# Optimization experiments

Hardware: AMD Instinct MI355X
Metric: run time of the kernel (lower is better)

Reference implementation:

```python
import jax, jax.numpy as jnp
import numpy as np

N = 20000      # nodes per snapshot
E = 160000     # edges per snapshot
T = 8          # timesteps
F_IN = 256     # nfeat
HEADS = 4      # GAT heads
C = 128        # nhid_graph (per-head GAT out, concat=False -> mean)
GH = 128       # nhid_gru
NC = 2         # nclass
NEG_SLOPE = 0.2


def setup_inputs() -> dict:
    key = jax.random.key(0)
    ks = jax.random.split(key, 16)
    s = 0.05
    return {
        "graph": jax.random.randint(ks[0], (T, 2, E), 0, N),
        "fts": jax.random.normal(ks[1], (T, N, F_IN), dtype=jnp.float32),
        "time_steps": T,
        # GATConv params (PyG-style): lin weight, att_src/att_dst, bias
        "W_gat": jax.random.normal(ks[2], (F_IN, HEADS * C), dtype=jnp.float32) * s,
        "att_src": jax.random.normal(ks[3], (HEADS, C), dtype=jnp.float32) * s,
        "att_dst": jax.random.normal(ks[4], (HEADS, C), dtype=jnp.float32) * s,
        "b_gat": jax.random.normal(ks[5], (C,), dtype=jnp.float32) * s,
        # GRU params (torch layout: [3H, in], gates order r,z,n)
        "W_ih": jax.random.normal(ks[6], (3 * GH, C), dtype=jnp.float32) * s,
        "W_hh": jax.random.normal(ks[7], (3 * GH, GH), dtype=jnp.float32) * s,
        "b_ih": jax.random.normal(ks[8], (3 * GH,), dtype=jnp.float32) * s,
        "b_hh": jax.random.normal(ks[9], (3 * GH,), dtype=jnp.float32) * s,
        # Attention ('general'): linear_in [H,H] no bias, linear_out [H,2H] no bias
        "W_att_in": jax.random.normal(ks[10], (GH, GH), dtype=jnp.float32) * s,
        "W_att_out": jax.random.normal(ks[11], (GH, 2 * GH), dtype=jnp.float32) * s,
        # final classifier
        "W_cls": jax.random.normal(ks[12], (NC, GH), dtype=jnp.float32) * s,
        "b_cls": jax.random.normal(ks[13], (NC,), dtype=jnp.float32) * s,
    }


def _segment_softmax(logits, seg, num_segments):
    # logits: [E', H], seg: [E'] destination node ids
    m = jax.ops.segment_max(logits, seg, num_segments=num_segments)
    m = jnp.where(jnp.isfinite(m), m, 0.0)
    e = jnp.exp(logits - m[seg])
    s = jax.ops.segment_sum(e, seg, num_segments=num_segments)
    return e / (s[seg] + 1e-16)


def _gat_step(x, edge_index, W_gat, att_src, att_dst, b_gat):
    # PyG GATConv: concat=False (mean over heads), negative_slope=0.2,
    # add_self_loops=True; eval mode so attention dropout is identity.
    n = x.shape[0]
    xw = (x @ W_gat).reshape(n, HEADS, C)                 # [N,H,C]
    loops = jnp.arange(n, dtype=edge_index.dtype)
    src = jnp.concatenate([edge_index[0], loops])         # [E']
    dst = jnp.concatenate([edge_index[1], loops])
    a_src = jnp.einsum('nhc,hc->nh', xw, att_src)         # [N,H]
    a_dst = jnp.einsum('nhc,hc->nh', xw, att_dst)
    alpha = jax.nn.leaky_relu(a_src[src] + a_dst[dst], NEG_SLOPE)  # [E',H]
    alpha = _segment_softmax(alpha, dst, n)
    msg = xw[src] * alpha[..., None]                      # [E',H,C]
    out = jax.ops.segment_sum(msg, dst, num_segments=n)   # [N,H,C]
    return out.mean(axis=1) + b_gat                       # [N,C]


def _gru(y, W_ih, W_hh, b_ih, b_hh):
    # y: [T, N, C]; torch GRU equations, h0 = 0
    n = y.shape[1]
    def step(h, x):
        gi = x @ W_ih.T + b_ih
        gh = h @ W_hh.T + b_hh
        i_r, i_z, i_n = jnp.split(gi, 3, axis=-1)
        h_r, h_z, h_n = jnp.split(gh, 3, axis=-1)
        r = jax.nn.sigmoid(i_r + h_r)
        z = jax.nn.sigmoid(i_z + h_z)
        nn_ = jnp.tanh(i_n + r * h_n)
        h_new = (1.0 - z) * nn_ + z * h
        return h_new, h_new
    h0 = jnp.zeros((n, GH), dtype=y.dtype)
    last, full = jax.lax.scan(step, h0, y)
    return full, last  # [T,N,GH], [N,GH]


def reference(graph, fts, time_steps, W_gat, att_src, att_dst, b_gat,
              W_ih, W_hh, b_ih, b_hh, W_att_in, W_att_out, W_cls, b_cls):
    # per-timestep GAT + leaky_relu(0.2)
    ys = [jax.nn.leaky_relu(
            _gat_step(fts[i], graph[i], W_gat, att_src, att_dst, b_gat),
            NEG_SLOPE)
          for i in range(time_steps)]
    y = jnp.stack(ys)                                     # [T,N,C]
    context, last = _gru(y, W_ih, W_hh, b_ih, b_hh)
    query = last[:, None, :]                              # [N,1,GH]
    context = jnp.transpose(context, (1, 0, 2))           # [N,T,GH]
    # Attention('general')
    q = query @ W_att_in.T                                # [N,1,GH]
    scores = jnp.einsum('nod,ntd->not', q, context)       # [N,1,T]
    w = jax.nn.softmax(scores, axis=-1)
    mix = jnp.einsum('not,ntd->nod', w, context)          # [N,1,GH]
    combined = jnp.concatenate([mix, q], axis=-1)         # [N,1,2GH]
    att_out = jnp.tanh(combined @ W_att_out.T)            # [N,1,GH]
    output = jax.nn.leaky_relu(att_out.reshape(-1, GH), NEG_SLOPE)
    logits = output @ W_cls.T + b_cls                     # [N,NC]
    return jax.nn.log_softmax(logits, axis=1)
```

## Files before the change

kernel.cpp:

```cpp
#include <hip/hip_runtime.h>
#include <hip/hip_bf16.h>
#include <math.h>

#define N_NODES 20000
#define N_EDGES 160000
#define T_STEPS 8
#define F_INC   256
#define HEADS   4
#define CCH     128
#define KC      512
#define GHD     128
#define G3      384
#define SLOPE   0.2f
#define SEG     (N_EDGES + N_NODES)

typedef unsigned short u16;
typedef __attribute__((ext_vector_type(8))) short bf16x8;
typedef __attribute__((ext_vector_type(4))) float f32x4;

__device__ __forceinline__ float leakyf(float x) { return x > 0.f ? x : SLOPE * x; }
__device__ __forceinline__ float b2f(u16 u) {
  union { unsigned int i; float f; } x; x.i = ((unsigned int)u) << 16; return x.f;
}
__device__ __forceinline__ u16 f2b(float f) {
  union { float f; unsigned int i; } u; u.f = f;
  unsigned int r = u.i + 0x7FFFu + ((u.i >> 16) & 1u);
  return (u16)(r >> 16);
}
__device__ __forceinline__ float sigf(float x) { return 1.f / (1.f + expf(-x)); }

__device__ __forceinline__ void gload16(const void* g, void* l) {
  __builtin_amdgcn_global_load_lds(
      (const __attribute__((address_space(1))) unsigned int*)g,
      (__attribute__((address_space(3))) unsigned int*)l, 16, 0, 0);
}

template <int OBF, int FUSE>
__global__ __launch_bounds__(256) void gemm_bf16(
    const u16* __restrict__ A, const u16* __restrict__ B,
    const float* __restrict__ bias, void* __restrict__ Cout,
    int M, int K, int Nt, int swz,
    const float* __restrict__ attS, const float* __restrict__ attD,
    float* __restrict__ asrc, float* __restrict__ adst)
{
  __shared__ u16 As[128][32];
  __shared__ u16 Bs[128][32];
  __shared__ float s_as[128], s_ad[128];
  const int tid  = threadIdx.x;
  const int wave = tid >> 6, lane = tid & 63;
  const int wr = (wave >> 1) * 64, wc = (wave & 1) * 64;
  int bx = blockIdx.x, by = blockIdx.y;
  if (swz) {
    const int gx = gridDim.x;
    const int nwg = gx * (int)gridDim.y;
    const int lin = by * gx + bx;
    const int q = nwg >> 3, r = nwg & 7;
    const int xcd = lin & 7, idx = lin >> 3;
    const int wg = (xcd < r ? xcd * (q + 1) : r * (q + 1) + (xcd - r) * q) + idx;
    bx = wg % gx; by = wg / gx;
  }
  const int bm = by * 128, bn = bx * 128;
  const int l15 = lane & 15, g = lane >> 4;

  if (FUSE && tid < 128) { s_as[tid] = 0.f; s_ad[tid] = 0.f; }

  const int sr = tid >> 2, sd = tid & 3;
  const int ss = sd ^ ((sr >> 1) & 3);
  const u16* aS0 = A + (size_t)min(bm + sr,      M - 1) * K + ss * 8;
  const u16* aS1 = A + (size_t)min(bm + 64 + sr, M - 1) * K + ss * 8;
  const u16* bS0 = B + (size_t)(bn + sr)      * K + ss * 8;
  const u16* bS1 = B + (size_t)(bn + 64 + sr) * K + ss * 8;
  u16* lA0 = &As[0][0] + (size_t)(tid & ~63) * 8;
  u16* lA1 = lA0 + 2048;
  u16* lB0 = &Bs[0][0] + (size_t)(tid & ~63) * 8;
  u16* lB1 = lB0 + 2048;

  f32x4 acc[4][4];
  #pragma unroll
  for (int m = 0; m < 4; ++m)
    #pragma unroll
    for (int n = 0; n < 4; ++n)
      #pragma unroll
      for (int j = 0; j < 4; ++j) acc[m][n][j] = 0.f;

  const int nK = K >> 5;
  for (int kt = 0; kt < nK; ++kt) {
    const int ko = kt * 32;
    gload16(aS0 + ko, lA0);
    gload16(aS1 + ko, lA1);
    gload16(bS0 + ko, lB0);
    gload16(bS1 + ko, lB1);
    __syncthreads();
    bf16x8 af[4], bfr[4];
    #pragma unroll
    for (int m = 0; m < 4; ++m) {
      int row = wr + m * 16 + l15;
      af[m] = *(const bf16x8*)&As[row][(g ^ ((row >> 1) & 3)) * 8];
      int rowb = wc + m * 16 + l15;
      bfr[m] = *(const bf16x8*)&Bs[rowb][(g ^ ((rowb >> 1) & 3)) * 8];
    }
    #pragma unroll
    for (int m = 0; m < 4; ++m)
      #pragma unroll
      for (int n = 0; n < 4; ++n)
        acc[m][n] = __builtin_amdgcn_mfma_f32_16x16x32_bf16(af[m], bfr[n], acc[m][n], 0, 0, 0);
    __syncthreads();
  }
  #pragma unroll
  for (int m = 0; m < 4; ++m) {
    int row0 = bm + wr + m * 16 + g * 4;
    #pragma unroll
    for (int n = 0; n < 4; ++n) {
      int col = bn + wc + n * 16 + l15;
      float bv = bias ? bias[col] : 0.f;
      #pragma unroll
      for (int j = 0; j < 4; ++j) {
        int row = row0 + j;
        if (row < M) {
          float v = acc[m][n][j] + bv;
          if (OBF) ((u16*)Cout)[(size_t)row * Nt + col] = f2b(v);
          else     ((float*)Cout)[(size_t)row * Nt + col] = v;
        }
      }
    }
  }
  if (FUSE) {
    float ps[4][4], pd[4][4];
    #pragma unroll
    for (int m = 0; m < 4; ++m)
      #pragma unroll
      for (int j = 0; j < 4; ++j) { ps[m][j] = 0.f; pd[m][j] = 0.f; }
    #pragma unroll
    for (int n = 0; n < 4; ++n) {
      int cl = wc + n * 16 + l15;
      float wsv = attS[bn + cl], wdv = attD[bn + cl];
      #pragma unroll
      for (int m = 0; m < 4; ++m)
        #pragma unroll
        for (int j = 0; j < 4; ++j) {
          ps[m][j] = fmaf(acc[m][n][j], wsv, ps[m][j]);
          pd[m][j] = fmaf(acc[m][n][j], wdv, pd[m][j]);
        }
    }
    #pragma unroll
    for (int m = 0; m < 4; ++m)
      #pragma unroll
      for (int j = 0; j < 4; ++j)
        #pragma unroll
        for (int msk = 8; msk >= 1; msk >>= 1) {
          ps[m][j] += __shfl_xor(ps[m][j], msk);
          pd[m][j] += __shfl_xor(pd[m][j], msk);
        }
    if (l15 == 0) {
      #pragma unroll
      for (int m = 0; m < 4; ++m)
        #pragma unroll
        for (int j = 0; j < 4; ++j) {
          atomicAdd(&s_as[wr + m * 16 + g * 4 + j], ps[m][j]);
          atomicAdd(&s_ad[wr + m * 16 + g * 4 + j], pd[m][j]);
        }
    }
    __syncthreads();
    if (tid < 128) {
      int row = bm + tid;
      if (row < M) {
        int h = bn >> 7;
        asrc[(size_t)row * 4 + h] = s_as[tid];
        adst[(size_t)row * 4 + h] = s_ad[tid];
      }
    }
  }
}

__global__ void convert_f32_bf16(const float* __restrict__ src, u16* __restrict__ dst, int n) {
  int i = (blockIdx.x * 256 + threadIdx.x) * 8;
  if (i >= n) return;
  float4 v0 = *(const float4*)(src + i);
  float4 v1 = *(const float4*)(src + i + 4);
  bf16x8 o;
  o[0] = (short)f2b(v0.x); o[1] = (short)f2b(v0.y);
  o[2] = (short)f2b(v0.z); o[3] = (short)f2b(v0.w);
  o[4] = (short)f2b(v1.x); o[5] = (short)f2b(v1.y);
  o[6] = (short)f2b(v1.z); o[7] = (short)f2b(v1.w);
  *(bf16x8*)(dst + i) = o;
}

__global__ void conv_transpose_wgat(const float* __restrict__ src, u16* __restrict__ dst) {
  int idx = blockIdx.x * 256 + threadIdx.x;
  if (idx >= KC * F_INC) return;
  int n = idx >> 8, k = idx & 255;
  dst[(size_t)n * F_INC + k] = f2b(src[(size_t)k * KC + n]);
}

__global__ void count_kernel(const int* __restrict__ graph, int* __restrict__ counts) {
  int e = blockIdx.x * 256 + threadIdx.x;
  int t = blockIdx.y;
  if (e < N_EDGES) {
    int d = graph[(size_t)t * 2 * N_EDGES + N_EDGES + e];
    atomicAdd(&counts[t * N_NODES + d], 1);
  }
}

__global__ __launch_bounds__(1024) void scan_kernel(
    const int* __restrict__ counts, int* __restrict__ offs)
{
  const int t = blockIdx.x;
  const int tid = threadIdx.x, lane = tid & 63, w = tid >> 6;
  __shared__ int s_wt[16];
  int carry = 0;
  const int base_abs = t * SEG;
  for (int base = 0; base < N_NODES; base += 1024) {
    int i = base + tid;
    int v = (i < N_NODES) ? (counts[t * N_NODES + i] + 1) : 0;
    int x = v;
    #pragma unroll
    for (int d = 1; d < 64; d <<= 1) {
      int nvl = __shfl_up(x, d, 64);
      if (lane >= d) x += nvl;
    }
    if (lane == 63) s_wt[w] = x;
    __syncthreads();
    if (tid < 16) {
      int y = s_wt[tid];
      #pragma unroll
      for (int d = 1; d < 16; d <<= 1) {
        int nvl = __shfl_up(y, d, 64);
        if (tid >= d) y += nvl;
      }
      s_wt[tid] = y;
    }
    __syncthreads();
    int wbase = (w > 0) ? s_wt[w - 1] : 0;
    int total = s_wt[15];
    if (i < N_NODES) offs[t * (N_NODES + 1) + i] = base_abs + carry + wbase + x - v;
    carry += total;
    __syncthreads();
  }
  if (tid == 0) offs[t * (N_NODES + 1) + N_NODES] = base_abs + carry;
}

__global__ void scatter_kernel(const int* __restrict__ graph, const int* __restrict__ offs,
                               int* __restrict__ cursor, int* __restrict__ ssrc)
{
  int i = blockIdx.x * 256 + threadIdx.x;
  int t = blockIdx.y;
  if (i >= SEG) return;
  int s, d;
  if (i < N_EDGES) {
    s = graph[(size_t)t * 2 * N_EDGES + i];
    d = graph[(size_t)t * 2 * N_EDGES + N_EDGES + i];
  } else {
    s = d = i - N_EDGES;
  }
  int pos = offs[t * (N_NODES + 1) + d] + atomicAdd(&cursor[t * N_NODES + d], 1);
  ssrc[pos] = s;
}

__global__ __launch_bounds__(256) void aggregate_kernel(
    const u16* __restrict__ xw, const float* __restrict__ a_src,
    const float* __restrict__ a_dst, const float* __restrict__ b_gat,
    const int* __restrict__ offs, const int* __restrict__ ssrc,
    u16* __restrict__ yout)
{
  const int wv = threadIdx.x >> 6, lane = threadIdx.x & 63;
  const int nd = blockIdx.x * 4 + wv;
  const int t  = blockIdx.y;
  __shared__ float s_w[4][64][4];
  __shared__ int   s_s[4][64];
  const int ob = t * (N_NODES + 1) + nd;
  const int beg = offs[ob], end = offs[ob + 1];
  const size_t rowbase = (size_t)t * N_NODES;
  const float4 adv = *(const float4*)&a_dst[(rowbase + nd) * 4];
  const int hl = lane >> 4;

  float m0=-INFINITY, m1=-INFINITY, m2=-INFINITY, m3=-INFINITY;
  float s0=0.f, s1=0.f, s2=0.f, s3=0.f;
  for (int base = beg; base < end; base += 64) {
    int e = base + lane;
    float a0=-INFINITY, a1=-INFINITY, a2=-INFINITY, a3=-INFINITY;
    if (e < end) {
      int s = ssrc[e];
      float4 av = *(const float4*)&a_src[(rowbase + s) * 4];
      a0 = leakyf(av.x + adv.x); a1 = leakyf(av.y + adv.y);
      a2 = leakyf(av.z + adv.z); a3 = leakyf(av.w + adv.w);
    }
    float c0=a0, c1=a1, c2=a2, c3=a3;
    #pragma unroll
    for (int msk = 32; msk >= 1; msk >>= 1) {
      c0 = fmaxf(c0, __shfl_xor(c0, msk)); c1 = fmaxf(c1, __shfl_xor(c1, msk));
      c2 = fmaxf(c2, __shfl_xor(c2, msk)); c3 = fmaxf(c3, __shfl_xor(c3, msk));
    }
    float n0 = fmaxf(m0, c0), n1 = fmaxf(m1, c1), n2 = fmaxf(m2, c2), n3 = fmaxf(m3, c3);
    float e0 = expf(a0 - n0), e1 = expf(a1 - n1), e2 = expf(a2 - n2), e3 = expf(a3 - n3);
    #pragma unroll
    for (int msk = 32; msk >= 1; msk >>= 1) {
      e0 += __shfl_xor(e0, msk); e1 += __shfl_xor(e1, msk);
      e2 += __shfl_xor(e2, msk); e3 += __shfl_xor(e3, msk);
    }
    s0 = s0 * expf(m0 - n0) + e0; s1 = s1 * expf(m1 - n1) + e1;
    s2 = s2 * expf(m2 - n2) + e2; s3 = s3 * expf(m3 - n3) + e3;
    m0 = n0; m1 = n1; m2 = n2; m3 = n3;
  }
  const float i0 = 1.f/(s0+1e-16f), i1 = 1.f/(s1+1e-16f);
  const float i2 = 1.f/(s2+1e-16f), i3 = 1.f/(s3+1e-16f);

  float acc[8] = {0.f,0.f,0.f,0.f,0.f,0.f,0.f,0.f};
  for (int base = beg; base < end; base += 64) {
    int e = base + lane;
    if (e < end) {
      int s = ssrc[e];
      float4 av = *(const float4*)&a_src[(rowbase + s) * 4];
      s_s[wv][lane] = s;
      s_w[wv][lane][0] = expf(leakyf(av.x + adv.x) - m0) * i0;
      s_w[wv][lane][1] = expf(leakyf(av.y + adv.y) - m1) * i1;
      s_w[wv][lane][2] = expf(leakyf(av.z + adv.z) - m2) * i2;
      s_w[wv][lane][3] = expf(leakyf(av.w + adv.w) - m3) * i3;
    }
    int cnt = min(64, end - base);
    for (int e2 = 0; e2 < cnt; ++e2) {
      float w = s_w[wv][e2][hl];
      const int4 xi = *(const int4*)&xw[(rowbase + s_s[wv][e2]) * KC + lane * 8];
      acc[0] = fmaf(w, b2f((u16)(xi.x & 0xffff)), acc[0]);
      acc[1] = fmaf(w, b2f((u16)((unsigned)xi.x >> 16)), acc[1]);
      acc[2] = fmaf(w, b2f((u16)(xi.y & 0xffff)), acc[2]);
      acc[3] = fmaf(w, b2f((u16)((unsigned)xi.y >> 16)), acc[3]);
      acc[4] = fmaf(w, b2f((u16)(xi.z & 0xffff)), acc[4]);
      acc[5] = fmaf(w, b2f((u16)((unsigned)xi.z >> 16)), acc[5]);
      acc[6] = fmaf(w, b2f((u16)(xi.w & 0xffff)), acc[6]);
      acc[7] = fmaf(w, b2f((u16)((unsigned)xi.w >> 16)), acc[7]);
    }
  }
  #pragma unroll
  for (int k = 0; k < 8; ++k) {
    acc[k] += __shfl_xor(acc[k], 16);
    acc[k] += __shfl_xor(acc[k], 32);
  }
  if (lane < 16) {
    bf16x8 ov;
    #pragma unroll
    for (int k = 0; k < 8; ++k) {
      float v = acc[k] * 0.25f + b_gat[lane * 8 + k];
      ov[k] = (short)f2b(leakyf(v));
    }
    *(bf16x8*)&yout[(rowbase + nd) * GHD + lane * 8] = ov;
  }
}

__global__ void gru_combine0(const u16* __restrict__ gi_t, const float* __restrict__ b_hh,
                             u16* __restrict__ ctx0, float* __restrict__ hf)
{
  int idx = blockIdx.x * 256 + threadIdx.x;
  if (idx >= N_NODES * GHD) return;
  int n = idx >> 7, c = idx & 127;
  size_t gb = (size_t)n * G3;
  float ir = b2f(gi_t[gb + c]), iz = b2f(gi_t[gb + 128 + c]), in_ = b2f(gi_t[gb + 256 + c]);
  float r = sigf(ir + b_hh[c]);
  float z = sigf(iz + b_hh[128 + c]);
  float nn = tanhf(in_ + r * b_hh[256 + c]);
  float h = (1.f - z) * nn;
  ctx0[idx] = f2b(h);
  hf[idx] = h;
}

__global__ __launch_bounds__(256) void gru_fused(
    const u16* __restrict__ hprev, const u16* __restrict__ Whh,
    const float* __restrict__ b_hh, const u16* __restrict__ gi_t,
    float* __restrict__ hf, u16* __restrict__ ctx_out)
{
  __shared__ u16 lds[64 * 384];
  u16 (*As)[32] = (u16(*)[32])lds;
  u16 (*Bs)[32] = (u16(*)[32])(lds + 64 * 32);
  const int tid = threadIdx.x, lane = tid & 63, wv = tid >> 6;
  const int l15 = lane & 15, g = lane >> 4;
  const int bm = blockIdx.x * 64;

  const int sr = tid >> 2, sd = tid & 3;
  const int ss = sd ^ ((sr >> 1) & 3);
  const u16* aS = hprev + (size_t)min(bm + sr, N_NODES - 1) * GHD + ss * 8;
  u16* lA = lds + (size_t)tid * 8 - (size_t)(lane & 63) * 8 + (size_t)(lane) * 8;
  lA = lds + (size_t)(tid & ~63) * 8;
  const u16* bS[6]; u16* lB[6];
  #pragma unroll
  for (int p = 0; p < 6; ++p) {
    int r = sr + p * 64;
    bS[p] = Whh + (size_t)r * GHD + ss * 8;
    lB[p] = lds + 64 * 32 + (size_t)(p * 256 + (tid & ~63)) * 8;
  }

  f32x4 acc[4][6];
  #pragma unroll
  for (int m = 0; m < 4; ++m)
    #pragma unroll
    for (int n = 0; n < 6; ++n)
      #pragma unroll
      for (int j = 0; j < 4; ++j) acc[m][n][j] = 0.f;

  #pragma unroll
  for (int kt = 0; kt < 4; ++kt) {
    const int ko = kt * 32;
    gload16(aS + ko, lA);
    #pragma unroll
    for (int p = 0; p < 6; ++p) gload16(bS[p] + ko, lB[p]);
    __syncthreads();
    bf16x8 af[4], bfr[6];
    #pragma unroll
    for (int m = 0; m < 4; ++m) {
      int row = m * 16 + l15;
      af[m] = *(const bf16x8*)&As[row][(g ^ ((row >> 1) & 3)) * 8];
    }
    #pragma unroll
    for (int n = 0; n < 6; ++n) {
      int row = wv * 96 + n * 16 + l15;
      bfr[n] = *(const bf16x8*)&Bs[row][(g ^ ((row >> 1) & 3)) * 8];
    }
    #pragma unroll
    for (int m = 0; m < 4; ++m)
      #pragma unroll
      for (int n = 0; n < 6; ++n)
        acc[m][n] = __builtin_amdgcn_mfma_f32_16x16x32_bf16(af[m], bfr[n], acc[m][n], 0, 0, 0);
    __syncthreads();
  }
  #pragma unroll
  for (int m = 0; m < 4; ++m)
    #pragma unroll
    for (int n = 0; n < 6; ++n) {
      int c = wv * 96 + n * 16 + l15;
      float bb = b_hh[c];
      #pragma unroll
      for (int j = 0; j < 4; ++j) {
        int r = m * 16 + g * 4 + j;
        lds[r * 384 + (((c >> 3) ^ (r & 7)) << 3) + (c & 7)] = f2b(acc[m][n][j] + bb);
      }
    }
  __syncthreads();
  {
    int r = tid >> 2, gr = bm + r;
    if (gr < N_NODES) {
      const int cg = (tid & 3) * 32;
      const size_t gb = (size_t)gr * G3;
      const size_t cb = (size_t)gr * GHD;
      #pragma unroll
      for (int q = 0; q < 4; ++q) {
        int c0 = cg + q * 8;
        int sl0 = ((c0 >> 3) ^ (r & 7));
        int sl1 = (((128 + c0) >> 3) ^ (r & 7));
        int sl2 = (((256 + c0) >> 3) ^ (r & 7));
        bf16x8 hr8 = *(bf16x8*)&lds[r * 384 + sl0 * 8];
        bf16x8 hz8 = *(bf16x8*)&lds[r * 384 + sl1 * 8];
        bf16x8 hn8 = *(bf16x8*)&lds[r * 384 + sl2 * 8];
        bf16x8 ir8 = *(const bf16x8*)&gi_t[gb + c0];
        bf16x8 iz8 = *(const bf16x8*)&gi_t[gb + 128 + c0];
        bf16x8 in8 = *(const bf16x8*)&gi_t[gb + 256 + c0];
        float4 hp0 = *(const float4*)&hf[cb + c0];
        float4 hp1 = *(const float4*)&hf[cb + c0 + 4];
        float hp[8] = {hp0.x, hp0.y, hp0.z, hp0.w, hp1.x, hp1.y, hp1.z, hp1.w};
        float cv[8];
        bf16x8 hv;
        #pragma unroll
        for (int k = 0; k < 8; ++k) {
          float rr = sigf(b2f((u16)ir8[k]) + b2f((u16)hr8[k]));
          float zz = sigf(b2f((u16)iz8[k]) + b2f((u16)hz8[k]));
          float nn = tanhf(b2f((u16)in8[k]) + rr * b2f((u16)hn8[k]));
          float h = (1.f - zz) * nn + zz * hp[k];
          cv[k] = h;
          hv[k] = (short)f2b(h);
        }
        *(float4*)&hf[cb + c0]     = make_float4(cv[0], cv[1], cv[2], cv[3]);
        *(float4*)&hf[cb + c0 + 4] = make_float4(cv[4], cv[5], cv[6], cv[7]);
        *(bf16x8*)&ctx_out[cb + c0] = hv;
      }
    }
  }
}

__global__ __launch_bounds__(256) void attn_mid(
    const u16* __restrict__ ctx, const float* __restrict__ q,
    u16* __restrict__ comb)
{
  const int node = blockIdx.x * 4 + (threadIdx.x >> 6);
  const int lane = threadIdx.x & 63;
  if (node >= N_NODES) return;
  const float q0 = q[(size_t)node * GHD + lane];
  const float q1 = q[(size_t)node * GHD + 64 + lane];
  float c0[T_STEPS], c1[T_STEPS], w[T_STEPS];
  float mx = -1e30f;
  #pragma unroll
  for (int t = 0; t < T_STEPS; ++t) {
    const u16* cr = ctx + ((size_t)t * N_NODES + node) * GHD;
    c0[t] = b2f(cr[lane]); c1[t] = b2f(cr[64 + lane]);
    float p = q0 * c0[t] + q1 * c1[t];
    #pragma unroll
    for (int m = 32; m >= 1; m >>= 1) p += __shfl_xor(p, m);
    w[t] = p;
    mx = fmaxf(mx, p);
  }
  float s = 0.f;
  #pragma unroll
  for (int t = 0; t < T_STEPS; ++t) { w[t] = expf(w[t] - mx); s += w[t]; }
  const float inv = 1.f / s;
  float m0 = 0.f, m1 = 0.f;
  #pragma unroll
  for (int t = 0; t < T_STEPS; ++t) { m0 = fmaf(w[t], c0[t], m0); m1 = fmaf(w[t], c1[t], m1); }
  m0 *= inv; m1 *= inv;
  u16* cb = comb + (size_t)node * 2 * GHD;
  cb[lane]       = f2b(m0);
  cb[64 + lane]  = f2b(m1);
  cb[128 + lane] = f2b(q0);
  cb[192 + lane] = f2b(q1);
}

__global__ __launch_bounds__(256) void logits_kernel(
    const u16* __restrict__ ao, const float* __restrict__ W_cls,
    const float* __restrict__ b_cls, float* __restrict__ out)
{
  const int node = blockIdx.x * 4 + (threadIdx.x >> 6);
  const int lane = threadIdx.x & 63;
  if (node >= N_NODES) return;
  float o0 = leakyf(tanhf(b2f(ao[(size_t)node * GHD + lane])));
  float o1 = leakyf(tanhf(b2f(ao[(size_t)node * GHD + 64 + lane])));
  float p0 = o0 * W_cls[lane] + o1 * W_cls[64 + lane];
  float p1 = o0 * W_cls[128 + lane] + o1 * W_cls[192 + lane];
  #pragma unroll
  for (int m = 32; m >= 1; m >>= 1) { p0 += __shfl_xor(p0, m); p1 += __shfl_xor(p1, m); }
  if (lane == 0) {
    float l0 = p0 + b_cls[0];
    float l1 = p1 + b_cls[1];
    float mx = fmaxf(l0, l1);
    float lse = mx + logf(expf(l0 - mx) + expf(l1 - mx));
    out[(size_t)node * 2 + 0] = l0 - lse;
    out[(size_t)node * 2 + 1] = l1 - lse;
  }
}

extern "C" void kernel_launch(void* const* d_in, const int* in_sizes, int n_in,
                              void* d_out, int out_size, void* d_ws, size_t ws_size,
                              hipStream_t stream)
{
  const int*   graph     = (const int*)  d_in[0];
  const float* fts       = (const float*)d_in[1];
  const float* W_gat     = (const float*)d_in[3];
  const float* att_src   = (const float*)d_in[4];
  const float* att_dst   = (const float*)d_in[5];
  const float* b_gat     = (const float*)d_in[6];
  const float* W_ih      = (const float*)d_in[7];
  const float* W_hh      = (const float*)d_in[8];
  const float* b_ih      = (const float*)d_in[9];
  const float* b_hh      = (const float*)d_in[10];
  const float* W_att_in  = (const float*)d_in[11];
  const float* W_att_out = (const float*)d_in[12];
  const float* W_cls     = (const float*)d_in[13];
  const float* b_cls     = (const float*)d_in[14];
  float* out = (float*)d_out;

  char* ws = (char*)d_ws;
  size_t off = 0;
  auto alloc = [&](size_t bytes) {
    void* p = ws + off;
    off = (off + bytes + 255) & ~(size_t)255;
    return p;
  };
  const size_t NT = (size_t)T_STEPS * N_NODES;
  u16*   wgatT = (u16*)alloc((size_t)KC * F_INC * 2);
  u16*   wihb  = (u16*)alloc((size_t)G3 * GHD * 2);
  u16*   whhb  = (u16*)alloc((size_t)G3 * GHD * 2);
  u16*   winb  = (u16*)alloc((size_t)GHD * GHD * 2);
  u16*   woutb = (u16*)alloc((size_t)GHD * 2 * GHD * 2);
  u16*   fbf   = (u16*)alloc(NT * F_INC * 2);
  u16*   xw    = (u16*)alloc(NT * KC * 2);
  float* asrc  = (float*)alloc(NT * 4 * 4);
  float* adst  = (float*)alloc(NT * 4 * 4);
  u16*   yall  = (u16*)alloc(NT * GHD * 2);
  u16*   giall = (u16*)alloc(NT * G3 * 2);
  u16*   ctx   = (u16*)alloc(NT * GHD * 2);
  float* hf    = (float*)alloc((size_t)N_NODES * GHD * 4);
  float* qf    = (float*)alloc((size_t)N_NODES * GHD * 4);
  u16*   comb  = (u16*)alloc((size_t)N_NODES * 2 * GHD * 2);
  u16*   aob   = (u16*)alloc((size_t)N_NODES * GHD * 2);
  int* counts  = (int*)alloc((size_t)2 * T_STEPS * N_NODES * 4);
  int* cursor  = counts + T_STEPS * N_NODES;
  int* offs    = (int*)alloc((size_t)T_STEPS * (N_NODES + 1) * 4);
  int* ssrc    = (int*)alloc((size_t)T_STEPS * SEG * 4);

  conv_transpose_wgat<<<dim3((KC * F_INC + 255) / 256), 256, 0, stream>>>(W_gat, wgatT);
  convert_f32_bf16<<<dim3(G3 * GHD / 8 / 256), 256, 0, stream>>>(W_ih, wihb, G3 * GHD);
  convert_f32_bf16<<<dim3(G3 * GHD / 8 / 256), 256, 0, stream>>>(W_hh, whhb, G3 * GHD);
  convert_f32_bf16<<<dim3(GHD * GHD / 8 / 256), 256, 0, stream>>>(W_att_in, winb, GHD * GHD);
  convert_f32_bf16<<<dim3(GHD * 2 * GHD / 8 / 256), 256, 0, stream>>>(W_att_out, woutb, GHD * 2 * GHD);

  hipMemsetAsync(counts, 0, (size_t)2 * T_STEPS * N_NODES * 4, stream);
  count_kernel<<<dim3(N_EDGES / 256, T_STEPS), 256, 0, stream>>>(graph, counts);
  scan_kernel<<<dim3(T_STEPS), 1024, 0, stream>>>(counts, offs);
  scatter_kernel<<<dim3((SEG + 255) / 256, T_STEPS), 256, 0, stream>>>(graph, offs, cursor, ssrc);

  convert_f32_bf16<<<dim3((int)(NT * F_INC / 8 / 256)), 256, 0, stream>>>(
      fts, fbf, (int)(NT * F_INC));

  gemm_bf16<1, 1><<<dim3(KC / 128, (int)(NT / 128)), 256, 0, stream>>>(
      fbf, wgatT, nullptr, xw, (int)NT, F_INC, KC, 1, att_src, att_dst, asrc, adst);

  aggregate_kernel<<<dim3(N_NODES / 4, T_STEPS), 256, 0, stream>>>(
      xw, asrc, adst, b_gat, offs, ssrc, yall);

  gemm_bf16<1, 0><<<dim3(G3 / 128, (int)(NT / 128)), 256, 0, stream>>>(
      yall, wihb, b_ih, giall, (int)NT, GHD, G3, 1, nullptr, nullptr, nullptr, nullptr);

  gru_combine0<<<dim3(N_NODES * GHD / 256), 256, 0, stream>>>(giall, b_hh, ctx, hf);
  for (int t = 1; t < T_STEPS; ++t) {
    gru_fused<<<dim3((N_NODES + 63) / 64), 256, 0, stream>>>(
        ctx + (size_t)(t - 1) * N_NODES * GHD, whhb, b_hh,
        giall + (size_t)t * N_NODES * G3, hf,
        ctx + (size_t)t * N_NODES * GHD);
  }

  gemm_bf16<0, 0><<<dim3(1, (N_NODES + 127) / 128), 256, 0, stream>>>(
      ctx + (size_t)(T_STEPS - 1) * N_NODES * GHD, winb, nullptr, qf,
      N_NODES, GHD, GHD, 0, nullptr, nullptr, nullptr, nullptr);
  attn_mid<<<dim3(N_NODES / 4), 256, 0, stream>>>(ctx, qf, comb);
  gemm_bf16<1, 0><<<dim3(1, (N_NODES + 127) / 128), 256, 0, stream>>>(
      comb, woutb, nullptr, aob, N_NODES, 2 * GHD, GHD, 0, nullptr, nullptr, nullptr, nullptr);
  logits_kernel<<<dim3(N_NODES / 4), 256, 0, stream>>>(aob, W_cls, b_cls, out);
}
```

Baseline: 838.9 us.

## Fuse GAT softmax and aggregation into one online pass with gather prefetch

The aggregate kernel now runs an online softmax. It rescales the running feature accumulators whenever the max changes and normalises once at the end, so the second pass over edges, with its reloads of ssrc and a_src and its recomputed exps, is gone. The gather of xw rows is software-pipelined with a four-deep register ring to hide memory latency, and the bf16 unpack uses shifts and masks. The four weight-conversion launches are merged into one kernel to cut launch overhead. The trade-off is an extra multiply on the accumulators per chunk, more registers, and slightly different floating-point rounding.

New measurement: 1.184 ms. 1.41x slower.

```diff
diff --git a/kernel.cpp b/kernel.cpp
--- a/kernel.cpp
+++ b/kernel.cpp
@@ -185,6 +185,28 @@
   *(bf16x8*)(dst + i) = o;
 }
 
+__global__ void convert_weights(const float* __restrict__ w_ih, const float* __restrict__ w_hh,
+                                const float* __restrict__ w_in, const float* __restrict__ w_out,
+                                u16* __restrict__ wihb, u16* __restrict__ whhb,
+                                u16* __restrict__ winb, u16* __restrict__ woutb)
+{
+  int i = blockIdx.x * 256 + threadIdx.x;
+  const float* src; u16* dst; int base;
+  if      (i < 6144)  { src = w_ih;  dst = wihb;  base = i; }
+  else if (i < 12288) { src = w_hh;  dst = whhb;  base = i - 6144; }
+  else if (i < 14336) { src = w_in;  dst = winb;  base = i - 12288; }
+  else                { src = w_out; dst = woutb; base = i - 14336; }
+  int o = base * 8;
+  float4 v0 = *(const float4*)(src + o);
+  float4 v1 = *(const float4*)(src + o + 4);
+  bf16x8 ov;
+  ov[0] = (short)f2b(v0.x); ov[1] = (short)f2b(v0.y);
+  ov[2] = (short)f2b(v0.z); ov[3] = (short)f2b(v0.w);
+  ov[4] = (short)f2b(v1.x); ov[5] = (short)f2b(v1.y);
+  ov[6] = (short)f2b(v1.z); ov[7] = (short)f2b(v1.w);
+  *(bf16x8*)(dst + o) = ov;
+}
+
 __global__ void conv_transpose_wgat(const float* __restrict__ src, u16* __restrict__ dst) {
   int idx = blockIdx.x * 256 + threadIdx.x;
   if (idx >= KC * F_INC) return;
@@ -275,11 +297,14 @@
 
   float m0=-INFINITY, m1=-INFINITY, m2=-INFINITY, m3=-INFINITY;
   float s0=0.f, s1=0.f, s2=0.f, s3=0.f;
+  float acc[8] = {0.f,0.f,0.f,0.f,0.f,0.f,0.f,0.f};
+
   for (int base = beg; base < end; base += 64) {
     int e = base + lane;
     float a0=-INFINITY, a1=-INFINITY, a2=-INFINITY, a3=-INFINITY;
     if (e < end) {
       int s = ssrc[e];
+      s_s[wv][lane] = s;
       float4 av = *(const float4*)&a_src[(rowbase + s) * 4];
       a0 = leakyf(av.x + adv.x); a1 = leakyf(av.y + adv.y);
       a2 = leakyf(av.z + adv.z); a3 = leakyf(av.w + adv.w);
@@ -291,47 +316,49 @@
       c2 = fmaxf(c2, __shfl_xor(c2, msk)); c3 = fmaxf(c3, __shfl_xor(c3, msk));
     }
     float n0 = fmaxf(m0, c0), n1 = fmaxf(m1, c1), n2 = fmaxf(m2, c2), n3 = fmaxf(m3, c3);
-    float e0 = expf(a0 - n0), e1 = expf(a1 - n1), e2 = expf(a2 - n2), e3 = expf(a3 - n3);
+    float sc0 = expf(m0 - n0), sc1 = expf(m1 - n1), sc2 = expf(m2 - n2), sc3 = expf(m3 - n3);
+    float sch = (hl == 0) ? sc0 : (hl == 1) ? sc1 : (hl == 2) ? sc2 : sc3;
+    #pragma unroll
+    for (int k = 0; k < 8; ++k) acc[k] *= sch;
+    float w0 = expf(a0 - n0), w1 = expf(a1 - n1), w2 = expf(a2 - n2), w3 = expf(a3 - n3);
+    s_w[wv][lane][0] = w0; s_w[wv][lane][1] = w1;
+    s_w[wv][lane][2] = w2; s_w[wv][lane][3] = w3;
+    float t0=w0, t1=w1, t2=w2, t3=w3;
     #pragma unroll
     for (int msk = 32; msk >= 1; msk >>= 1) {
-      e0 += __shfl_xor(e0, msk); e1 += __shfl_xor(e1, msk);
-      e2 += __shfl_xor(e2, msk); e3 += __shfl_xor(e3, msk);
-    }
-    s0 = s0 * expf(m0 - n0) + e0; s1 = s1 * expf(m1 - n1) + e1;
-    s2 = s2 * expf(m2 - n2) + e2; s3 = s3 * expf(m3 - n3) + e3;
+      t0 += __shfl_xor(t0, msk); t1 += __shfl_xor(t1, msk);
+      t2 += __shfl_xor(t2, msk); t3 += __shfl_xor(t3, msk);
+    }
+    s0 = s0 * sc0 + t0; s1 = s1 * sc1 + t1;
+    s2 = s2 * sc2 + t2; s3 = s3 * sc3 + t3;
     m0 = n0; m1 = n1; m2 = n2; m3 = n3;
-  }
-  const float i0 = 1.f/(s0+1e-16f), i1 = 1.f/(s1+1e-16f);
-  const float i2 = 1.f/(s2+1e-16f), i3 = 1.f/(s3+1e-16f);
-
-  float acc[8] = {0.f,0.f,0.f,0.f,0.f,0.f,0.f,0.f};
-  for (int base = beg; base < end; base += 64) {
-    int e = base + lane;
-    if (e < end) {
-      int s = ssrc[e];
-      float4 av = *(const float4*)&a_src[(rowbase + s) * 4];
-      s_s[wv][lane] = s;
-      s_w[wv][lane][0] = expf(leakyf(av.x + adv.x) - m0) * i0;
-      s_w[wv][lane][1] = expf(leakyf(av.y + adv.y) - m1) * i1;
-      s_w[wv][lane][2] = expf(leakyf(av.z + adv.z) - m2) * i2;
-      s_w[wv][lane][3] = expf(leakyf(av.w + adv.w) - m3) * i3;
-    }
+
     int cnt = min(64, end - base);
+    int4 buf[4];
+    #pragma unroll
+    for (int j = 0; j < 4; ++j)
+      if (j < cnt)
+        buf[j] = *(const int4*)&xw[(rowbase + s_s[wv][j]) * KC + lane * 8];
     for (int e2 = 0; e2 < cnt; ++e2) {
+      int4 xi = buf[e2 & 3];
+      if (e2 + 4 < cnt)
+        buf[e2 & 3] = *(const int4*)&xw[(rowbase + s_s[wv][e2 + 4]) * KC + lane * 8];
       float w = s_w[wv][e2][hl];
-      const int4 xi = *(const int4*)&xw[(rowbase + s_s[wv][e2]) * KC + lane * 8];
-      acc[0] = fmaf(w, b2f((u16)(xi.x & 0xffff)), acc[0]);
-      acc[1] = fmaf(w, b2f((u16)((unsigned)xi.x >> 16)), acc[1]);
-      acc[2] = fmaf(w, b2f((u16)(xi.y & 0xffff)), acc[2]);
-      acc[3] = fmaf(w, b2f((u16)((unsigned)xi.y >> 16)), acc[3]);
-      acc[4] = fmaf(w, b2f((u16)(xi.z & 0xffff)), acc[4]);
-      acc[5] = fmaf(w, b2f((u16)((unsigned)xi.z >> 16)), acc[5]);
-      acc[6] = fmaf(w, b2f((u16)(xi.w & 0xffff)), acc[6]);
-      acc[7] = fmaf(w, b2f((u16)((unsigned)xi.w >> 16)), acc[7]);
-    }
-  }
+      acc[0] = fmaf(w, __uint_as_float((unsigned)xi.x << 16), acc[0]);
+      acc[1] = fmaf(w, __uint_as_float((unsigned)xi.x & 0xffff0000u), acc[1]);
+      acc[2] = fmaf(w, __uint_as_float((unsigned)xi.y << 16), acc[2]);
+      acc[3] = fmaf(w, __uint_as_float((unsigned)xi.y & 0xffff0000u), acc[3]);
+      acc[4] = fmaf(w, __uint_as_float((unsigned)xi.z << 16), acc[4]);
+      acc[5] = fmaf(w, __uint_as_float((unsigned)xi.z & 0xffff0000u), acc[5]);
+      acc[6] = fmaf(w, __uint_as_float((unsigned)xi.w << 16), acc[6]);
+      acc[7] = fmaf(w, __uint_as_float((unsigned)xi.w & 0xffff0000u), acc[7]);
+    }
+  }
+  float sh = (hl == 0) ? s0 : (hl == 1) ? s1 : (hl == 2) ? s2 : s3;
+  float inv = 1.f / (sh + 1e-16f);
   #pragma unroll
   for (int k = 0; k < 8; ++k) {
+    acc[k] *= inv;
     acc[k] += __shfl_xor(acc[k], 16);
     acc[k] += __shfl_xor(acc[k], 32);
   }
@@ -377,8 +404,7 @@
   const int sr = tid >> 2, sd = tid & 3;
   const int ss = sd ^ ((sr >> 1) & 3);
   const u16* aS = hprev + (size_t)min(bm + sr, N_NODES - 1) * GHD + ss * 8;
-  u16* lA = lds + (size_t)tid * 8 - (size_t)(lane & 63) * 8 + (size_t)(lane) * 8;
-  lA = lds + (size_t)(tid & ~63) * 8;
+  u16* lA = lds + (size_t)(tid & ~63) * 8;
   const u16* bS[6]; u16* lB[6];
   #pragma unroll
   for (int p = 0; p < 6; ++p) {
@@ -582,10 +608,8 @@
   int* ssrc    = (int*)alloc((size_t)T_STEPS * SEG * 4);
 
   conv_transpose_wgat<<<dim3((KC * F_INC + 255) / 256), 256, 0, stream>>>(W_gat, wgatT);
-  convert_f32_bf16<<<dim3(G3 * GHD / 8 / 256), 256, 0, stream>>>(W_ih, wihb, G3 * GHD);
-  convert_f32_bf16<<<dim3(G3 * GHD / 8 / 256), 256, 0, stream>>>(W_hh, whhb, G3 * GHD);
-  convert_f32_bf16<<<dim3(GHD * GHD / 8 / 256), 256, 0, stream>>>(W_att_in, winb, GHD * GHD);
-  convert_f32_bf16<<<dim3(GHD * 2 * GHD / 8 / 256), 256, 0, stream>>>(W_att_out, woutb, GHD * 2 * GHD);
+  convert_weights<<<dim3(72), 256, 0, stream>>>(W_ih, W_hh, W_att_in, W_att_out,
+                                                wihb, whhb, winb, woutb);
 
   hipMemsetAsync(counts, 0, (size_t)2 * T_STEPS * N_NODES * 4, stream);
   count_kernel<<<dim3(N_EDGES / 256, T_STEPS), 256, 0, stream>>>(graph, counts);
```
